# Kernel optimization log

Measured on AMD Instinct MI355X. Metric: run time of the kernel, lower is better.

The kernel has to match this reference:

```python
import jax, jax.numpy as jnp
import numpy as np
import math

B, S, D, H = 4, 2048, 1024, 16
HD = D // H  # head_size = 64


def setup_inputs() -> dict:
    key = jax.random.key(0)
    ks = jax.random.split(key, 12)
    s = 1.0 / math.sqrt(D)
    inp = {
        "query_in": jax.random.normal(ks[0], (B, S, D), jnp.float32),
        "key_in": jax.random.normal(ks[1], (B, S, D), jnp.float32),
        "values_in": jax.random.normal(ks[2], (B, S, D), jnp.float32),
        # causal mask, broadcast over batch and heads
        "mask": jnp.tril(jnp.ones((S, S), jnp.int32))[None, None],
        "Wq": jax.random.normal(ks[3], (D, D), jnp.float32) * s,
        "bq": jnp.zeros((D,), jnp.float32),
        "Wk": jax.random.normal(ks[4], (D, D), jnp.float32) * s,
        "bk": jnp.zeros((D,), jnp.float32),
        "Wv": jax.random.normal(ks[5], (D, D), jnp.float32) * s,
        "bv": jnp.zeros((D,), jnp.float32),
        "Wo": jax.random.normal(ks[6], (D, D), jnp.float32) * s,
        "bo": jnp.zeros((D,), jnp.float32),
    }
    return inp


def _heads(x):
    # [B,S,D] -> [B,H,S,HD]
    return x.reshape(B, S, H, HD).transpose(0, 2, 1, 3)


def reference(query_in, key_in, values_in, mask, Wq, bq, Wk, bk, Wv, bv, Wo, bo):
    q = _heads(query_in @ Wq.T + bq)
    k = _heads(key_in @ Wk.T + bk)
    v = _heads(values_in @ Wv.T + bv)
    # scaled dot-product scores [B,H,Sq,Sk]
    att = jnp.einsum("bhqd,bhkd->bhqk", q, k) / math.sqrt(HD)
    att = jnp.where(mask == 0, jnp.float32(-1e9), att)
    # NOTE: original module applies dropout (identity at eval / p=0) directly
    # to scores with NO softmax -- faithfully reproduced here.
    out = jnp.einsum("bhqk,bhkd->bhqd", att, v)
    out = out.transpose(0, 2, 1, 3).reshape(B, S, D)
    return out @ Wo.T + bo
```

## Files before the change

### kernel.cpp

```cpp
#include <hip/hip_runtime.h>
#include <stdint.h>

typedef unsigned short ushort_t;
typedef __bf16 bf16x8 __attribute__((ext_vector_type(8)));
typedef float f32x4 __attribute__((ext_vector_type(4)));
typedef ushort_t us4 __attribute__((ext_vector_type(4)));

#define MFMA16(a, b, c) __builtin_amdgcn_mfma_f32_16x16x32_bf16((a), (b), (c), 0, 0, 0)

constexpr int Bn = 4, Sn = 2048, Dn = 1024, Hn = 16, HDn = 64;
constexpr float SCALE = 0.125f;
constexpr float NEG = -1e9f;

__device__ __forceinline__ float bf2f(ushort_t u) {
  unsigned x = ((unsigned)u) << 16;
  return __builtin_bit_cast(float, x);
}
__device__ __forceinline__ ushort_t f2bf(float f) {
  unsigned x = __builtin_bit_cast(unsigned, f);
  x = x + 0x7FFFu + ((x >> 16) & 1u);
  return (ushort_t)(x >> 16);
}
__device__ __forceinline__ uint4 ld8_f32_bf16(const float* __restrict__ p) {
  float4 a = *(const float4*)p;
  float4 b = *(const float4*)(p + 4);
  union { ushort_t u[8]; uint4 v; } r;
  r.u[0] = f2bf(a.x); r.u[1] = f2bf(a.y); r.u[2] = f2bf(a.z); r.u[3] = f2bf(a.w);
  r.u[4] = f2bf(b.x); r.u[5] = f2bf(b.y); r.u[6] = f2bf(b.z); r.u[7] = f2bf(b.w);
  return r.v;
}
__device__ __forceinline__ void gl2lds16(const void* g, void* l) {
  __builtin_amdgcn_global_load_lds(
      (__attribute__((address_space(1))) void*)g,
      (__attribute__((address_space(3))) void*)l, 16, 0, 0);
}

__global__ __launch_bounds__(256)
void cvt2(const float* __restrict__ X, ushort_t* __restrict__ Xd,
          const float* __restrict__ W, ushort_t* __restrict__ Wd) {
  int bid = blockIdx.x;
  if (bid < 512) {
    size_t i = ((size_t)bid * 256 + threadIdx.x) * 8;
    *(uint4*)(Wd + i) = ld8_f32_bf16(W + i);
  } else {
    size_t i = ((size_t)(bid - 512) * 256 + threadIdx.x) * 8;
    *(uint4*)(Xd + i) = ld8_f32_bf16(X + i);
  }
}
__global__ __launch_bounds__(256)
void cvt1(const float* __restrict__ s, ushort_t* __restrict__ d) {
  size_t i = ((size_t)blockIdx.x * 256 + threadIdx.x) * 8;
  *(uint4*)(d + i) = ld8_f32_bf16(s + i);
}

template <int EPI>
__global__ __launch_bounds__(256)
void gemm_bt(const ushort_t* __restrict__ A, const ushort_t* __restrict__ Wt,
             const float* __restrict__ bias, void* __restrict__ Cp) {
  constexpr int K = 1024;
  __shared__ __align__(16) ushort_t As[128 * 64];
  __shared__ __align__(16) ushort_t Bs[128 * 64];

  const int tid = threadIdx.x;
  const int lane = tid & 63, w = tid >> 6;
  const int quad = lane >> 4, l16 = lane & 15;
  const int wm = w >> 1, wn = w & 1;
  const int row0 = blockIdx.y * 128;
  const int col0 = blockIdx.x * 128;

  const int sr = lane >> 3;
  const int sg = ((lane & 7) ^ (sr & 7)) * 8;
  const ushort_t* Ab = A  + (size_t)(row0 + w * 32 + sr) * K + sg;
  const ushort_t* Bb = Wt + (size_t)(col0 + w * 32 + sr) * K + sg;

  f32x4 acc[4][4] = {};

  for (int k0 = 0; k0 < K; k0 += 64) {
    __syncthreads();
#pragma unroll
    for (int i = 0; i < 4; ++i) {
      gl2lds16(Ab + (size_t)(i * 8) * K + k0, &As[(w * 32 + i * 8) * 64]);
      gl2lds16(Bb + (size_t)(i * 8) * K + k0, &Bs[(w * 32 + i * 8) * 64]);
    }
    __syncthreads();
#pragma unroll
    for (int ks = 0; ks < 2; ++ks) {
      const int kg = ((ks * 4 + quad) ^ (l16 & 7)) * 8;
      bf16x8 af[4], bfr[4];
#pragma unroll
      for (int mt = 0; mt < 4; ++mt)
        af[mt] = *(const bf16x8*)(&As[(wm * 64 + mt * 16 + l16) * 64 + kg]);
#pragma unroll
      for (int nt = 0; nt < 4; ++nt)
        bfr[nt] = *(const bf16x8*)(&Bs[(wn * 64 + nt * 16 + l16) * 64 + kg]);
#pragma unroll
      for (int mt = 0; mt < 4; ++mt)
#pragma unroll
        for (int nt = 0; nt < 4; ++nt)
          acc[mt][nt] = MFMA16(af[mt], bfr[nt], acc[mt][nt]);
    }
  }

#pragma unroll
  for (int mt = 0; mt < 4; ++mt) {
#pragma unroll
    for (int nt = 0; nt < 4; ++nt) {
      const int col = col0 + wn * 64 + nt * 16 + l16;
      const float bv = bias[col];
      const int rowb = row0 + wm * 64 + mt * 16 + quad * 4;
      if (EPI == 1) {
        const int b = rowb >> 11, s = rowb & (Sn - 1);
        const int h = col >> 6, hd = col & 63;
        us4 pk;
#pragma unroll
        for (int r = 0; r < 4; ++r) pk[r] = f2bf(acc[mt][nt][r] + bv);
        *(us4*)((ushort_t*)Cp + ((size_t)((b * Hn + h) * HDn + hd)) * Sn + s) = pk;
      } else {
#pragma unroll
        for (int r = 0; r < 4; ++r) {
          const int row = rowb + r;
          const float outv = acc[mt][nt][r] + bv;
          if (EPI == 2) {
            ((float*)Cp)[(size_t)row * 1024 + col] = outv;
          } else {
            const int b = row >> 11, s = row & (Sn - 1);
            const int h = col >> 6, hd = col & 63;
            ((ushort_t*)Cp)[(((size_t)(b * Hn + h) * Sn + s) << 6) + hd] = f2bf(outv);
          }
        }
      }
    }
  }
}

__global__ __launch_bounds__(64)
void tilesum64(const ushort_t* __restrict__ Vt, float* __restrict__ tsum) {
  const int bh = blockIdx.x, t = blockIdx.y, n = threadIdx.x;
  const ushort_t* p = Vt + ((size_t)bh * HDn + n) * Sn + t * 64;
  float acc = 0.f;
#pragma unroll
  for (int j = 0; j < 8; ++j) {
    union { uint4 v; ushort_t u[8]; } c;
    c.v = *(const uint4*)(p + j * 8);
#pragma unroll
    for (int e = 0; e < 8; ++e) acc += bf2f(c.u[e]);
  }
  tsum[((size_t)bh * 32 + t) * 64 + n] = acc;
}

__global__ __launch_bounds__(64)
void suffix64(const float* __restrict__ tsum, float* __restrict__ suffV) {
  const int bh = blockIdx.x, n = threadIdx.x;
  float acc = 0.f;
  suffV[((size_t)bh * 32 + 31) * 64 + n] = 0.f;
  for (int t = 30; t >= 0; --t) {
    acc += tsum[((size_t)bh * 32 + t + 1) * 64 + n];
    suffV[((size_t)bh * 32 + t) * 64 + n] = acc;
  }
}

__global__ __launch_bounds__(256)
void prefixz(const ushort_t* __restrict__ Kt, const ushort_t* __restrict__ Vt,
             ushort_t* __restrict__ Zp) {
  __shared__ __align__(16) ushort_t Kts[64 * 64];
  __shared__ __align__(16) ushort_t Vts[64 * 64];
  const int tid = threadIdx.x, lane = tid & 63, w = tid >> 6;
  const int quad = lane >> 4, l16 = lane & 15;
  const int bh = blockIdx.x;
  const ushort_t* Ktb = Kt + (size_t)bh * HDn * Sn;
  const ushort_t* Vtb = Vt + (size_t)bh * HDn * Sn;

  const int sr = lane >> 3;
  const int sg = ((lane & 7) ^ (sr & 7)) * 8;

  f32x4 zacc[4] = {};

  for (int t = 0; t < 32; ++t) {
    __syncthreads();
#pragma unroll
    for (int c = 0; c < 2; ++c) {
      const int row = w * 16 + c * 8;
      gl2lds16(Ktb + (size_t)(row + sr) * Sn + t * 64 + sg, &Kts[row * 64]);
      gl2lds16(Vtb + (size_t)(row + sr) * Sn + t * 64 + sg, &Vts[row * 64]);
    }
    __syncthreads();
    ushort_t* zd = Zp + (size_t)(bh * 32 + t) * 4096;
#pragma unroll
    for (int nt = 0; nt < 4; ++nt) {
      us4 pk;
#pragma unroll
      for (int r = 0; r < 4; ++r) pk[r] = f2bf(SCALE * zacc[nt][r]);
      *(us4*)(zd + (nt * 16 + l16) * 64 + w * 16 + quad * 4) = pk;
    }
    if (t < 31) {
#pragma unroll
      for (int ks = 0; ks < 2; ++ks) {
        const int kg = ((ks * 4 + quad) ^ (l16 & 7)) * 8;
        bf16x8 ak = *(const bf16x8*)(&Kts[(w * 16 + l16) * 64 + kg]);
#pragma unroll
        for (int nt = 0; nt < 4; ++nt) {
          bf16x8 bv = *(const bf16x8*)(&Vts[(nt * 16 + l16) * 64 + kg]);
          zacc[nt] = MFMA16(ak, bv, zacc[nt]);
        }
      }
    }
  }
}

__global__ __launch_bounds__(256)
void attn_kernel(const ushort_t* __restrict__ Q, const ushort_t* __restrict__ Kt,
                 const ushort_t* __restrict__ Vt, const ushort_t* __restrict__ Zp,
                 const float* __restrict__ suffV, ushort_t* __restrict__ O) {
  __shared__ __align__(16) ushort_t Qs[64 * 64];
  __shared__ __align__(16) ushort_t Vts[64 * 64];
  __shared__ __align__(16) ushort_t Zs[64 * 64];
  __shared__ __align__(16) ushort_t Ks[64 * 64];
  __shared__ __align__(16) ushort_t Ss[64][72];

  const int tid = threadIdx.x, lane = tid & 63, w = tid >> 6;
  const int quad = lane >> 4, l16 = lane & 15;
  const int bh = blockIdx.y;
  const int qt = blockIdx.x;
  const int q0 = qt * 64;
  const int b = bh >> 4, h = bh & 15;
  const ushort_t* Qb  = Q  + (size_t)bh * Sn * HDn;
  const ushort_t* Ktb = Kt + (size_t)bh * HDn * Sn;
  const ushort_t* Vtb = Vt + (size_t)bh * HDn * Sn;
  const ushort_t* Zb  = Zp + (size_t)(bh * 32 + qt) * 4096;

  const int sr = lane >> 3;
  const int sg = ((lane & 7) ^ (sr & 7)) * 8;

#pragma unroll
  for (int c = 0; c < 2; ++c) {
    const int row = w * 16 + c * 8;
    gl2lds16(Qb + (size_t)(q0 + row + sr) * HDn + sg, &Qs[row * 64]);
    gl2lds16(Vtb + (size_t)(row + sr) * Sn + q0 + sg, &Vts[row * 64]);
    gl2lds16(Zb + (size_t)(row + sr) * 64 + sg, &Zs[row * 64]);
  }
  const int q8 = lane & 7, h8 = lane >> 3;
#pragma unroll
  for (int c = 0; c < 2; ++c) {
    const int hd = w * 16 + c * 8 + h8;
    const int G = hd >> 3;
    union { uint4 v; ushort_t u[8]; } kv;
    kv.v = *(const uint4*)(Ktb + (size_t)hd * Sn + q0 + q8 * 8);
#pragma unroll
    for (int j = 0; j < 8; ++j) {
      const int e = (j + q8) & 7;
      const int s = q8 * 8 + e;
      Ks[s * 64 + ((G ^ e) << 3) + (hd & 7)] = kv.u[e];
    }
  }
  __syncthreads();

  bf16x8 bq[2];
#pragma unroll
  for (int ks = 0; ks < 2; ++ks)
    bq[ks] = *(const bf16x8*)(&Qs[(w * 16 + l16) * 64 + (((ks * 4 + quad) ^ (l16 & 7)) << 3)]);

  f32x4 oacc[4] = {};
#pragma unroll
  for (int ks = 0; ks < 2; ++ks) {
    const int kg = ((ks * 4 + quad) ^ (l16 & 7)) * 8;
#pragma unroll
    for (int nt = 0; nt < 4; ++nt) {
      bf16x8 az = *(const bf16x8*)(&Zs[(nt * 16 + l16) * 64 + kg]);
      oacc[nt] = MFMA16(az, bq[ks], oacc[nt]);
    }
  }
  f32x4 sacc[4] = {};
#pragma unroll
  for (int ks = 0; ks < 2; ++ks) {
    const int kg = ((ks * 4 + quad) ^ (l16 & 7)) * 8;
#pragma unroll
    for (int nt = 0; nt < 4; ++nt) {
      bf16x8 ak = *(const bf16x8*)(&Ks[(nt * 16 + l16) * 64 + kg]);
      sacc[nt] = MFMA16(ak, bq[ks], sacc[nt]);
    }
  }
  const int qrel = w * 16 + l16;
#pragma unroll
  for (int nt = 0; nt < 4; ++nt) {
    const int kb = nt * 16 + quad * 4;
    us4 pk;
#pragma unroll
    for (int r = 0; r < 4; ++r) {
      float val = (kb + r > qrel) ? NEG : sacc[nt][r] * SCALE;
      pk[r] = f2bf(val);
    }
    *(us4*)(&Ss[qrel][kb]) = pk;
  }
#pragma unroll
  for (int ks = 0; ks < 2; ++ks) {
    bf16x8 bs = *(const bf16x8*)(&Ss[qrel][ks * 32 + quad * 8]);
#pragma unroll
    for (int nt = 0; nt < 4; ++nt) {
      bf16x8 av = *(const bf16x8*)(&Vts[(nt * 16 + l16) * 64 + (((ks * 4 + quad) ^ (l16 & 7)) << 3)]);
      oacc[nt] = MFMA16(av, bs, oacc[nt]);
    }
  }

  const float* sv = suffV + (size_t)(bh * 32 + qt) * 64;
  const int s = q0 + w * 16 + l16;
#pragma unroll
  for (int nt = 0; nt < 4; ++nt) {
    const int nb = nt * 16 + quad * 4;
    float4 s4 = *(const float4*)(sv + nb);
    us4 pk;
    pk[0] = f2bf(oacc[nt][0] + NEG * s4.x);
    pk[1] = f2bf(oacc[nt][1] + NEG * s4.y);
    pk[2] = f2bf(oacc[nt][2] + NEG * s4.z);
    pk[3] = f2bf(oacc[nt][3] + NEG * s4.w);
    *(us4*)(&O[((size_t)(b * Sn + s)) * Dn + h * 64 + nb]) = pk;
  }
}

extern "C" void kernel_launch(void* const* d_in, const int* in_sizes, int n_in,
                              void* d_out, int out_size, void* d_ws, size_t ws_size,
                              hipStream_t stream) {
  const float* Xq = (const float*)d_in[0];
  const float* Xk = (const float*)d_in[1];
  const float* Xv = (const float*)d_in[2];
  const float* Wq = (const float*)d_in[4];
  const float* bq = (const float*)d_in[5];
  const float* Wk = (const float*)d_in[6];
  const float* bk = (const float*)d_in[7];
  const float* Wv = (const float*)d_in[8];
  const float* bv = (const float*)d_in[9];
  const float* Wo = (const float*)d_in[10];
  const float* bo = (const float*)d_in[11];

  constexpr size_t MiB = 1024 * 1024;
  char* ws = (char*)d_ws;
  ushort_t* Xb  = (ushort_t*)(ws);
  ushort_t* Zp  = (ushort_t*)(ws);
  ushort_t* Qb  = (ushort_t*)(ws + 16 * MiB);
  ushort_t* Ktb = (ushort_t*)(ws + 32 * MiB);
  ushort_t* Vtb = (ushort_t*)(ws + 48 * MiB);
  ushort_t* Ob  = (ushort_t*)(ws + 64 * MiB);
  ushort_t* Wb  = (ushort_t*)(ws + 80 * MiB);
  float*    ts  = (float*)   (ws + 82 * MiB);
  float*    sV  = (float*)   (ws + 82 * MiB + 512 * 1024);

  const dim3 gg(8, 64), bb(256);
  cvt2<<<4608, 256, 0, stream>>>(Xq, Xb, Wq, Wb);
  gemm_bt<0><<<gg, bb, 0, stream>>>(Xb, Wb, bq, Qb);
  cvt2<<<4608, 256, 0, stream>>>(Xk, Xb, Wk, Wb);
  gemm_bt<1><<<gg, bb, 0, stream>>>(Xb, Wb, bk, Ktb);
  cvt2<<<4608, 256, 0, stream>>>(Xv, Xb, Wv, Wb);
  gemm_bt<1><<<gg, bb, 0, stream>>>(Xb, Wb, bv, Vtb);
  tilesum64<<<dim3(64, 32), 64, 0, stream>>>(Vtb, ts);
  suffix64<<<64, 64, 0, stream>>>(ts, sV);
  prefixz<<<64, 256, 0, stream>>>(Ktb, Vtb, Zp);
  attn_kernel<<<dim3(32, 64), 256, 0, stream>>>(Qb, Ktb, Vtb, Zp, sV, Ob);
  cvt1<<<512, 256, 0, stream>>>(Wo, Wb);
  gemm_bt<2><<<gg, bb, 0, stream>>>(Ob, Wb, bo, (float*)d_out);
}
```

Baseline: 348.5 us.

## Batch conversions and QKV GEMMs, fuse V suffix sums, double-buffer prefix and attention

All seven fp32-to-bf16 conversions now run in one launch, and the Q/K/V projections run as a single GEMM launch with a z grid dimension. The V tile-sum and suffix-scan kernels are folded into prefixz. Both prefixz and the attention kernel now double-buffer their LDS tiles, and each attention block processes four query tiles in a loop. This removes several small launches and serialization points and overlaps global loads with compute, at the cost of a larger workspace, more LDS per block and fewer attention blocks.

After: 330.5 us. -5.2%, faster.

```diff
diff --git a/kernel.cpp b/kernel.cpp
--- a/kernel.cpp
+++ b/kernel.cpp
@@ -36,30 +36,39 @@
 }
 
 __global__ __launch_bounds__(256)
-void cvt2(const float* __restrict__ X, ushort_t* __restrict__ Xd,
-          const float* __restrict__ W, ushort_t* __restrict__ Wd) {
-  int bid = blockIdx.x;
-  if (bid < 512) {
-    size_t i = ((size_t)bid * 256 + threadIdx.x) * 8;
-    *(uint4*)(Wd + i) = ld8_f32_bf16(W + i);
+void cvt_all(const float* __restrict__ xq, const float* __restrict__ xk,
+             const float* __restrict__ xv, const float* __restrict__ wq,
+             const float* __restrict__ wk, const float* __restrict__ wv,
+             const float* __restrict__ wo, ushort_t* __restrict__ Xd,
+             ushort_t* __restrict__ Wd) {
+  const int bid = blockIdx.x;
+  if (bid < 12288) {
+    const int which = bid >> 12;
+    const float* s = which == 0 ? xq : which == 1 ? xk : xv;
+    size_t i = ((size_t)(bid & 4095) * 256 + threadIdx.x) * 8;
+    *(uint4*)(Xd + (size_t)which * 8388608 + i) = ld8_f32_bf16(s + i);
   } else {
-    size_t i = ((size_t)(bid - 512) * 256 + threadIdx.x) * 8;
-    *(uint4*)(Xd + i) = ld8_f32_bf16(X + i);
-  }
-}
+    const int wb = bid - 12288, which = wb >> 9;
+    const float* s = which == 0 ? wq : which == 1 ? wk : which == 2 ? wv : wo;
+    size_t i = ((size_t)(wb & 511) * 256 + threadIdx.x) * 8;
+    *(uint4*)(Wd + (size_t)which * 1048576 + i) = ld8_f32_bf16(s + i);
+  }
+}
+
 __global__ __launch_bounds__(256)
-void cvt1(const float* __restrict__ s, ushort_t* __restrict__ d) {
-  size_t i = ((size_t)blockIdx.x * 256 + threadIdx.x) * 8;
-  *(uint4*)(d + i) = ld8_f32_bf16(s + i);
-}
-
-template <int EPI>
-__global__ __launch_bounds__(256)
-void gemm_bt(const ushort_t* __restrict__ A, const ushort_t* __restrict__ Wt,
-             const float* __restrict__ bias, void* __restrict__ Cp) {
+void gemm_qkv(const ushort_t* __restrict__ Xb, const ushort_t* __restrict__ Wb,
+              const float* __restrict__ bq, const float* __restrict__ bk,
+              const float* __restrict__ bv, ushort_t* __restrict__ Qd,
+              ushort_t* __restrict__ Ktd, ushort_t* __restrict__ Vtd) {
   constexpr int K = 1024;
   __shared__ __align__(16) ushort_t As[128 * 64];
   __shared__ __align__(16) ushort_t Bs[128 * 64];
+
+  const int z = blockIdx.z;
+  const ushort_t* A  = Xb + (size_t)z * 8388608;
+  const ushort_t* Wt = Wb + (size_t)z * 1048576;
+  const float* bias = z == 0 ? bq : z == 1 ? bk : bv;
+  ushort_t* Cp = z == 0 ? Qd : z == 1 ? Ktd : Vtd;
 
   const int tid = threadIdx.x;
   const int lane = tid & 63, w = tid >> 6;
@@ -106,64 +115,94 @@
 #pragma unroll
     for (int nt = 0; nt < 4; ++nt) {
       const int col = col0 + wn * 64 + nt * 16 + l16;
-      const float bv = bias[col];
+      const float bv4 = bias[col];
       const int rowb = row0 + wm * 64 + mt * 16 + quad * 4;
-      if (EPI == 1) {
+      if (z != 0) {
         const int b = rowb >> 11, s = rowb & (Sn - 1);
         const int h = col >> 6, hd = col & 63;
         us4 pk;
 #pragma unroll
-        for (int r = 0; r < 4; ++r) pk[r] = f2bf(acc[mt][nt][r] + bv);
-        *(us4*)((ushort_t*)Cp + ((size_t)((b * Hn + h) * HDn + hd)) * Sn + s) = pk;
+        for (int r = 0; r < 4; ++r) pk[r] = f2bf(acc[mt][nt][r] + bv4);
+        *(us4*)(Cp + ((size_t)((b * Hn + h) * HDn + hd)) * Sn + s) = pk;
       } else {
 #pragma unroll
         for (int r = 0; r < 4; ++r) {
           const int row = rowb + r;
-          const float outv = acc[mt][nt][r] + bv;
-          if (EPI == 2) {
-            ((float*)Cp)[(size_t)row * 1024 + col] = outv;
-          } else {
-            const int b = row >> 11, s = row & (Sn - 1);
-            const int h = col >> 6, hd = col & 63;
-            ((ushort_t*)Cp)[(((size_t)(b * Hn + h) * Sn + s) << 6) + hd] = f2bf(outv);
-          }
+          const int b = row >> 11, s = row & (Sn - 1);
+          const int h = col >> 6, hd = col & 63;
+          Cp[(((size_t)(b * Hn + h) * Sn + s) << 6) + hd] = f2bf(acc[mt][nt][r] + bv4);
         }
       }
     }
   }
 }
 
-__global__ __launch_bounds__(64)
-void tilesum64(const ushort_t* __restrict__ Vt, float* __restrict__ tsum) {
-  const int bh = blockIdx.x, t = blockIdx.y, n = threadIdx.x;
-  const ushort_t* p = Vt + ((size_t)bh * HDn + n) * Sn + t * 64;
-  float acc = 0.f;
-#pragma unroll
-  for (int j = 0; j < 8; ++j) {
-    union { uint4 v; ushort_t u[8]; } c;
-    c.v = *(const uint4*)(p + j * 8);
-#pragma unroll
-    for (int e = 0; e < 8; ++e) acc += bf2f(c.u[e]);
-  }
-  tsum[((size_t)bh * 32 + t) * 64 + n] = acc;
-}
-
-__global__ __launch_bounds__(64)
-void suffix64(const float* __restrict__ tsum, float* __restrict__ suffV) {
-  const int bh = blockIdx.x, n = threadIdx.x;
-  float acc = 0.f;
-  suffV[((size_t)bh * 32 + 31) * 64 + n] = 0.f;
-  for (int t = 30; t >= 0; --t) {
-    acc += tsum[((size_t)bh * 32 + t + 1) * 64 + n];
-    suffV[((size_t)bh * 32 + t) * 64 + n] = acc;
-  }
+__global__ __launch_bounds__(256)
+void gemm_out(const ushort_t* __restrict__ A, const ushort_t* __restrict__ Wt,
+              const float* __restrict__ bias, float* __restrict__ Cp) {
+  constexpr int K = 1024;
+  __shared__ __align__(16) ushort_t As[128 * 64];
+  __shared__ __align__(16) ushort_t Bs[128 * 64];
+
+  const int tid = threadIdx.x;
+  const int lane = tid & 63, w = tid >> 6;
+  const int quad = lane >> 4, l16 = lane & 15;
+  const int wm = w >> 1, wn = w & 1;
+  const int row0 = blockIdx.y * 128;
+  const int col0 = blockIdx.x * 128;
+
+  const int sr = lane >> 3;
+  const int sg = ((lane & 7) ^ (sr & 7)) * 8;
+  const ushort_t* Ab = A  + (size_t)(row0 + w * 32 + sr) * K + sg;
+  const ushort_t* Bb = Wt + (size_t)(col0 + w * 32 + sr) * K + sg;
+
+  f32x4 acc[4][4] = {};
+
+  for (int k0 = 0; k0 < K; k0 += 64) {
+    __syncthreads();
+#pragma unroll
+    for (int i = 0; i < 4; ++i) {
+      gl2lds16(Ab + (size_t)(i * 8) * K + k0, &As[(w * 32 + i * 8) * 64]);
+      gl2lds16(Bb + (size_t)(i * 8) * K + k0, &Bs[(w * 32 + i * 8) * 64]);
+    }
+    __syncthreads();
+#pragma unroll
+    for (int ks = 0; ks < 2; ++ks) {
+      const int kg = ((ks * 4 + quad) ^ (l16 & 7)) * 8;
+      bf16x8 af[4], bfr[4];
+#pragma unroll
+      for (int mt = 0; mt < 4; ++mt)
+        af[mt] = *(const bf16x8*)(&As[(wm * 64 + mt * 16 + l16) * 64 + kg]);
+#pragma unroll
+      for (int nt = 0; nt < 4; ++nt)
+        bfr[nt] = *(const bf16x8*)(&Bs[(wn * 64 + nt * 16 + l16) * 64 + kg]);
+#pragma unroll
+      for (int mt = 0; mt < 4; ++mt)
+#pragma unroll
+        for (int nt = 0; nt < 4; ++nt)
+          acc[mt][nt] = MFMA16(af[mt], bfr[nt], acc[mt][nt]);
+    }
+  }
+
+#pragma unroll
+  for (int mt = 0; mt < 4; ++mt)
+#pragma unroll
+    for (int nt = 0; nt < 4; ++nt) {
+      const int col = col0 + wn * 64 + nt * 16 + l16;
+      const float bv = bias[col];
+      const int rowb = row0 + wm * 64 + mt * 16 + quad * 4;
+#pragma unroll
+      for (int r = 0; r < 4; ++r)
+        Cp[(size_t)(rowb + r) * 1024 + col] = acc[mt][nt][r] + bv;
+    }
 }
 
 __global__ __launch_bounds__(256)
 void prefixz(const ushort_t* __restrict__ Kt, const ushort_t* __restrict__ Vt,
-             ushort_t* __restrict__ Zp) {
-  __shared__ __align__(16) ushort_t Kts[64 * 64];
-  __shared__ __align__(16) ushort_t Vts[64 * 64];
+             ushort_t* __restrict__ Zp, float* __restrict__ suffV) {
+  __shared__ __align__(16) ushort_t Kts[2][4096];
+  __shared__ __align__(16) ushort_t Vts[2][4096];
+  __shared__ float tsum[32 * 64];
   const int tid = threadIdx.x, lane = tid & 63, w = tid >> 6;
   const int quad = lane >> 4, l16 = lane & 15;
   const int bh = blockIdx.x;
@@ -173,17 +212,28 @@
   const int sr = lane >> 3;
   const int sg = ((lane & 7) ^ (sr & 7)) * 8;
 
+  for (int i = tid; i < 2048; i += 256) tsum[i] = 0.f;
+
+#pragma unroll
+  for (int c = 0; c < 2; ++c) {
+    const int row = w * 16 + c * 8;
+    gl2lds16(Ktb + (size_t)(row + sr) * Sn + sg, &Kts[0][row * 64]);
+    gl2lds16(Vtb + (size_t)(row + sr) * Sn + sg, &Vts[0][row * 64]);
+  }
+
   f32x4 zacc[4] = {};
 
   for (int t = 0; t < 32; ++t) {
-    __syncthreads();
-#pragma unroll
-    for (int c = 0; c < 2; ++c) {
-      const int row = w * 16 + c * 8;
-      gl2lds16(Ktb + (size_t)(row + sr) * Sn + t * 64 + sg, &Kts[row * 64]);
-      gl2lds16(Vtb + (size_t)(row + sr) * Sn + t * 64 + sg, &Vts[row * 64]);
-    }
-    __syncthreads();
+    const int cur = t & 1;
+    __syncthreads();
+    if (t < 31) {
+#pragma unroll
+      for (int c = 0; c < 2; ++c) {
+        const int row = w * 16 + c * 8;
+        gl2lds16(Ktb + (size_t)(row + sr) * Sn + (t + 1) * 64 + sg, &Kts[1 - cur][row * 64]);
+        gl2lds16(Vtb + (size_t)(row + sr) * Sn + (t + 1) * 64 + sg, &Vts[1 - cur][row * 64]);
+      }
+    }
     ushort_t* zd = Zp + (size_t)(bh * 32 + t) * 4096;
 #pragma unroll
     for (int nt = 0; nt < 4; ++nt) {
@@ -196,13 +246,34 @@
 #pragma unroll
       for (int ks = 0; ks < 2; ++ks) {
         const int kg = ((ks * 4 + quad) ^ (l16 & 7)) * 8;
-        bf16x8 ak = *(const bf16x8*)(&Kts[(w * 16 + l16) * 64 + kg]);
+        bf16x8 ak = *(const bf16x8*)(&Kts[cur][(w * 16 + l16) * 64 + kg]);
 #pragma unroll
         for (int nt = 0; nt < 4; ++nt) {
-          bf16x8 bv = *(const bf16x8*)(&Vts[(nt * 16 + l16) * 64 + kg]);
-          zacc[nt] = MFMA16(ak, bv, zacc[nt]);
+          bf16x8 bv8 = *(const bf16x8*)(&Vts[cur][(nt * 16 + l16) * 64 + kg]);
+          zacc[nt] = MFMA16(ak, bv8, zacc[nt]);
         }
       }
+    }
+    {
+      const int n = tid & 63, j = tid >> 6;
+      float p = 0.f;
+#pragma unroll
+      for (int gg2 = 0; gg2 < 2; ++gg2) {
+        const int g = 2 * j + gg2;
+        union { uint4 v; ushort_t u[8]; } c;
+        c.v = *(const uint4*)(&Vts[cur][n * 64 + ((g ^ (n & 7)) << 3)]);
+#pragma unroll
+        for (int e = 0; e < 8; ++e) p += bf2f(c.u[e]);
+      }
+      atomicAdd(&tsum[t * 64 + n], p);
+    }
+  }
+  __syncthreads();
+  if (tid < 64) {
+    float acc = 0.f;
+    for (int t = 31; t >= 0; --t) {
+      suffV[(size_t)(bh * 32 + t) * 64 + tid] = acc;
+      acc += tsum[t * 64 + tid];
     }
   }
 }
@@ -211,108 +282,130 @@
 void attn_kernel(const ushort_t* __restrict__ Q, const ushort_t* __restrict__ Kt,
                  const ushort_t* __restrict__ Vt, const ushort_t* __restrict__ Zp,
                  const float* __restrict__ suffV, ushort_t* __restrict__ O) {
-  __shared__ __align__(16) ushort_t Qs[64 * 64];
-  __shared__ __align__(16) ushort_t Vts[64 * 64];
-  __shared__ __align__(16) ushort_t Zs[64 * 64];
-  __shared__ __align__(16) ushort_t Ks[64 * 64];
+  __shared__ __align__(16) ushort_t Qs[2][4096];
+  __shared__ __align__(16) ushort_t Vts[2][4096];
+  __shared__ __align__(16) ushort_t Zs[2][4096];
+  __shared__ __align__(16) ushort_t Ks[2][4096];
   __shared__ __align__(16) ushort_t Ss[64][72];
 
   const int tid = threadIdx.x, lane = tid & 63, w = tid >> 6;
   const int quad = lane >> 4, l16 = lane & 15;
   const int bh = blockIdx.y;
-  const int qt = blockIdx.x;
-  const int q0 = qt * 64;
+  const int qtb = blockIdx.x * 4;
   const int b = bh >> 4, h = bh & 15;
   const ushort_t* Qb  = Q  + (size_t)bh * Sn * HDn;
   const ushort_t* Ktb = Kt + (size_t)bh * HDn * Sn;
   const ushort_t* Vtb = Vt + (size_t)bh * HDn * Sn;
-  const ushort_t* Zb  = Zp + (size_t)(bh * 32 + qt) * 4096;
 
   const int sr = lane >> 3;
   const int sg = ((lane & 7) ^ (sr & 7)) * 8;
-
-#pragma unroll
-  for (int c = 0; c < 2; ++c) {
-    const int row = w * 16 + c * 8;
-    gl2lds16(Qb + (size_t)(q0 + row + sr) * HDn + sg, &Qs[row * 64]);
-    gl2lds16(Vtb + (size_t)(row + sr) * Sn + q0 + sg, &Vts[row * 64]);
-    gl2lds16(Zb + (size_t)(row + sr) * 64 + sg, &Zs[row * 64]);
-  }
   const int q8 = lane & 7, h8 = lane >> 3;
-#pragma unroll
-  for (int c = 0; c < 2; ++c) {
-    const int hd = w * 16 + c * 8 + h8;
-    const int G = hd >> 3;
-    union { uint4 v; ushort_t u[8]; } kv;
-    kv.v = *(const uint4*)(Ktb + (size_t)hd * Sn + q0 + q8 * 8);
-#pragma unroll
-    for (int j = 0; j < 8; ++j) {
-      const int e = (j + q8) & 7;
-      const int s = q8 * 8 + e;
-      Ks[s * 64 + ((G ^ e) << 3) + (hd & 7)] = kv.u[e];
-    }
-  }
-  __syncthreads();
-
-  bf16x8 bq[2];
-#pragma unroll
-  for (int ks = 0; ks < 2; ++ks)
-    bq[ks] = *(const bf16x8*)(&Qs[(w * 16 + l16) * 64 + (((ks * 4 + quad) ^ (l16 & 7)) << 3)]);
-
-  f32x4 oacc[4] = {};
-#pragma unroll
-  for (int ks = 0; ks < 2; ++ks) {
-    const int kg = ((ks * 4 + quad) ^ (l16 & 7)) * 8;
+
+  uint4 kv[2];
+  {
+    const int q0 = qtb * 64;
+    const ushort_t* Zb = Zp + (size_t)(bh * 32 + qtb) * 4096;
+#pragma unroll
+    for (int c = 0; c < 2; ++c) {
+      const int row = w * 16 + c * 8;
+      gl2lds16(Qb + (size_t)(q0 + row + sr) * HDn + sg, &Qs[0][row * 64]);
+      gl2lds16(Vtb + (size_t)(row + sr) * Sn + q0 + sg, &Vts[0][row * 64]);
+      gl2lds16(Zb + (size_t)(row + sr) * 64 + sg, &Zs[0][row * 64]);
+      kv[c] = *(const uint4*)(Ktb + (size_t)(w * 16 + c * 8 + h8) * Sn + q0 + q8 * 8);
+    }
+  }
+
+  for (int i = 0; i < 4; ++i) {
+    const int cur = i & 1;
+    const int qt = qtb + i, q0 = qt * 64;
+
+#pragma unroll
+    for (int c = 0; c < 2; ++c) {
+      const int hd = w * 16 + c * 8 + h8;
+      const int G = hd >> 3;
+      const ushort_t* ku = (const ushort_t*)&kv[c];
+#pragma unroll
+      for (int j = 0; j < 8; ++j) {
+        const int e = (j + q8) & 7;
+        const int s = q8 * 8 + e;
+        Ks[cur][s * 64 + ((G ^ e) << 3) + (hd & 7)] = ku[e];
+      }
+    }
+    __syncthreads();
+
+    if (i < 3) {
+      const int q1 = (qt + 1) * 64;
+      const ushort_t* Zb = Zp + (size_t)(bh * 32 + qt + 1) * 4096;
+#pragma unroll
+      for (int c = 0; c < 2; ++c) {
+        const int row = w * 16 + c * 8;
+        gl2lds16(Qb + (size_t)(q1 + row + sr) * HDn + sg, &Qs[1 - cur][row * 64]);
+        gl2lds16(Vtb + (size_t)(row + sr) * Sn + q1 + sg, &Vts[1 - cur][row * 64]);
+        gl2lds16(Zb + (size_t)(row + sr) * 64 + sg, &Zs[1 - cur][row * 64]);
+        kv[c] = *(const uint4*)(Ktb + (size_t)(w * 16 + c * 8 + h8) * Sn + q1 + q8 * 8);
+      }
+    }
+
+    bf16x8 bq[2];
+#pragma unroll
+    for (int ks = 0; ks < 2; ++ks)
+      bq[ks] = *(const bf16x8*)(&Qs[cur][(w * 16 + l16) * 64 + (((ks * 4 + quad) ^ (l16 & 7)) << 3)]);
+
+    f32x4 oacc[4] = {};
+#pragma unroll
+    for (int ks = 0; ks < 2; ++ks) {
+      const int kg = ((ks * 4 + quad) ^ (l16 & 7)) * 8;
+#pragma unroll
+      for (int nt = 0; nt < 4; ++nt) {
+        bf16x8 az = *(const bf16x8*)(&Zs[cur][(nt * 16 + l16) * 64 + kg]);
+        oacc[nt] = MFMA16(az, bq[ks], oacc[nt]);
+      }
+    }
+    f32x4 sacc[4] = {};
+#pragma unroll
+    for (int ks = 0; ks < 2; ++ks) {
+      const int kg = ((ks * 4 + quad) ^ (l16 & 7)) * 8;
+#pragma unroll
+      for (int nt = 0; nt < 4; ++nt) {
+        bf16x8 ak = *(const bf16x8*)(&Ks[cur][(nt * 16 + l16) * 64 + kg]);
+        sacc[nt] = MFMA16(ak, bq[ks], sacc[nt]);
+      }
+    }
+    const int qrel = w * 16 + l16;
 #pragma unroll
     for (int nt = 0; nt < 4; ++nt) {
-      bf16x8 az = *(const bf16x8*)(&Zs[(nt * 16 + l16) * 64 + kg]);
-      oacc[nt] = MFMA16(az, bq[ks], oacc[nt]);
-    }
-  }
-  f32x4 sacc[4] = {};
-#pragma unroll
-  for (int ks = 0; ks < 2; ++ks) {
-    const int kg = ((ks * 4 + quad) ^ (l16 & 7)) * 8;
+      const int kb = nt * 16 + quad * 4;
+      us4 pk;
+#pragma unroll
+      for (int r = 0; r < 4; ++r) {
+        float val = (kb + r > qrel) ? NEG : sacc[nt][r] * SCALE;
+        pk[r] = f2bf(val);
+      }
+      *(us4*)(&Ss[qrel][kb]) = pk;
+    }
+#pragma unroll
+    for (int ks = 0; ks < 2; ++ks) {
+      bf16x8 bs = *(const bf16x8*)(&Ss[qrel][ks * 32 + quad * 8]);
+#pragma unroll
+      for (int nt = 0; nt < 4; ++nt) {
+        bf16x8 av = *(const bf16x8*)(&Vts[cur][(nt * 16 + l16) * 64 + (((ks * 4 + quad) ^ (l16 & 7)) << 3)]);
+        oacc[nt] = MFMA16(av, bs, oacc[nt]);
+      }
+    }
+
+    const float* sv = suffV + (size_t)(bh * 32 + qt) * 64;
+    const int s = q0 + w * 16 + l16;
 #pragma unroll
     for (int nt = 0; nt < 4; ++nt) {
-      bf16x8 ak = *(const bf16x8*)(&Ks[(nt * 16 + l16) * 64 + kg]);
-      sacc[nt] = MFMA16(ak, bq[ks], sacc[nt]);
-    }
-  }
-  const int qrel = w * 16 + l16;
-#pragma unroll
-  for (int nt = 0; nt < 4; ++nt) {
-    const int kb = nt * 16 + quad * 4;
-    us4 pk;
-#pragma unroll
-    for (int r = 0; r < 4; ++r) {
-      float val = (kb + r > qrel) ? NEG : sacc[nt][r] * SCALE;
-      pk[r] = f2bf(val);
-    }
-    *(us4*)(&Ss[qrel][kb]) = pk;
-  }
-#pragma unroll
-  for (int ks = 0; ks < 2; ++ks) {
-    bf16x8 bs = *(const bf16x8*)(&Ss[qrel][ks * 32 + quad * 8]);
-#pragma unroll
-    for (int nt = 0; nt < 4; ++nt) {
-      bf16x8 av = *(const bf16x8*)(&Vts[(nt * 16 + l16) * 64 + (((ks * 4 + quad) ^ (l16 & 7)) << 3)]);
-      oacc[nt] = MFMA16(av, bs, oacc[nt]);
-    }
-  }
-
-  const float* sv = suffV + (size_t)(bh * 32 + qt) * 64;
-  const int s = q0 + w * 16 + l16;
-#pragma unroll
-  for (int nt = 0; nt < 4; ++nt) {
-    const int nb = nt * 16 + quad * 4;
-    float4 s4 = *(const float4*)(sv + nb);
-    us4 pk;
-    pk[0] = f2bf(oacc[nt][0] + NEG * s4.x);
-    pk[1] = f2bf(oacc[nt][1] + NEG * s4.y);
-    pk[2] = f2bf(oacc[nt][2] + NEG * s4.z);
-    pk[3] = f2bf(oacc[nt][3] + NEG * s4.w);
-    *(us4*)(&O[((size_t)(b * Sn + s)) * Dn + h * 64 + nb]) = pk;
+      const int nb = nt * 16 + quad * 4;
+      float4 s4 = *(const float4*)(sv + nb);
+      us4 pk;
+      pk[0] = f2bf(oacc[nt][0] + NEG * s4.x);
+      pk[1] = f2bf(oacc[nt][1] + NEG * s4.y);
+      pk[2] = f2bf(oacc[nt][2] + NEG * s4.z);
+      pk[3] = f2bf(oacc[nt][3] + NEG * s4.w);
+      *(us4*)(&O[((size_t)(b * Sn + s)) * Dn + h * 64 + nb]) = pk;
+    }
   }
 }
 
@@ -334,26 +427,18 @@
   constexpr size_t MiB = 1024 * 1024;
   char* ws = (char*)d_ws;
   ushort_t* Xb  = (ushort_t*)(ws);
-  ushort_t* Zp  = (ushort_t*)(ws);
-  ushort_t* Qb  = (ushort_t*)(ws + 16 * MiB);
-  ushort_t* Ktb = (ushort_t*)(ws + 32 * MiB);
-  ushort_t* Vtb = (ushort_t*)(ws + 48 * MiB);
-  ushort_t* Ob  = (ushort_t*)(ws + 64 * MiB);
-  ushort_t* Wb  = (ushort_t*)(ws + 80 * MiB);
-  float*    ts  = (float*)   (ws + 82 * MiB);
-  float*    sV  = (float*)   (ws + 82 * MiB + 512 * 1024);
-
-  const dim3 gg(8, 64), bb(256);
-  cvt2<<<4608, 256, 0, stream>>>(Xq, Xb, Wq, Wb);
-  gemm_bt<0><<<gg, bb, 0, stream>>>(Xb, Wb, bq, Qb);
-  cvt2<<<4608, 256, 0, stream>>>(Xk, Xb, Wk, Wb);
-  gemm_bt<1><<<gg, bb, 0, stream>>>(Xb, Wb, bk, Ktb);
-  cvt2<<<4608, 256, 0, stream>>>(Xv, Xb, Wv, Wb);
-  gemm_bt<1><<<gg, bb, 0, stream>>>(Xb, Wb, bv, Vtb);
-  tilesum64<<<dim3(64, 32), 64, 0, stream>>>(Vtb, ts);
-  suffix64<<<64, 64, 0, stream>>>(ts, sV);
-  prefixz<<<64, 256, 0, stream>>>(Ktb, Vtb, Zp);
-  attn_kernel<<<dim3(32, 64), 256, 0, stream>>>(Qb, Ktb, Vtb, Zp, sV, Ob);
-  cvt1<<<512, 256, 0, stream>>>(Wo, Wb);
-  gemm_bt<2><<<gg, bb, 0, stream>>>(Ob, Wb, bo, (float*)d_out);
-}
+  ushort_t* Wb  = (ushort_t*)(ws + 48 * MiB);
+  ushort_t* Qb  = (ushort_t*)(ws + 56 * MiB);
+  ushort_t* Ktb = (ushort_t*)(ws + 72 * MiB);
+  ushort_t* Vtb = (ushort_t*)(ws + 88 * MiB);
+  ushort_t* Zp  = (ushort_t*)(ws + 104 * MiB);
+  ushort_t* Ob  = (ushort_t*)(ws + 120 * MiB);
+  float*    sV  = (float*)   (ws + 136 * MiB);
+
+  cvt_all<<<14336, 256, 0, stream>>>(Xq, Xk, Xv, Wq, Wk, Wv, Wo, Xb, Wb);
+  gemm_qkv<<<dim3(8, 64, 3), 256, 0, stream>>>(Xb, Wb, bq, bk, bv, Qb, Ktb, Vtb);
+  prefixz<<<64, 256, 0, stream>>>(Ktb, Vtb, Zp, sV);
+  attn_kernel<<<dim3(8, 64), 256, 0, stream>>>(Qb, Ktb, Vtb, Zp, sV, Ob);
+  gemm_out<<<dim3(8, 64), 256, 0, stream>>>(Ob, Wb + (size_t)3 * 1048576, bo,
+                                            (float*)d_out);
+}
```
